# Kernel tuning notes

Hardware: AMD Instinct MI355X
Metric: run time of the kernel (lower is better)

The kernel has to match this reference:

```python
import jax, jax.numpy as jnp
import numpy as np

N_NODES = 100000
N_EDGES = 1600000
D_IN = 128
D_HID = 128


def setup_inputs() -> dict:
    key = jax.random.key(0)
    ks = jax.random.split(key, 9)
    x = jax.random.normal(ks[0], (N_NODES, D_IN), dtype=jnp.float32)
    edge_index = jax.random.randint(ks[1], (2, N_EDGES), 0, N_NODES, dtype=jnp.int64)
    s = 1.0 / np.sqrt(D_IN)
    W0 = jax.random.uniform(ks[2], (D_IN, D_HID), jnp.float32, -s, s)
    W1 = jax.random.uniform(ks[3], (D_HID, D_HID), jnp.float32, -s, s)
    W2 = jax.random.uniform(ks[4], (D_HID, D_HID), jnp.float32, -s, s)
    b0 = jax.random.uniform(ks[5], (D_HID,), jnp.float32, -s, s)
    b1 = jax.random.uniform(ks[6], (D_HID,), jnp.float32, -s, s)
    b2 = jax.random.uniform(ks[7], (D_HID,), jnp.float32, -s, s)
    return {"x": x, "edge_index": edge_index,
            "W0": W0, "W1": W1, "W2": W2, "b0": b0, "b1": b1, "b2": b2}


def _gcn_norm(edge_index, num_nodes):
    # add self loops, compute symmetric normalization D^-1/2 (A+I) D^-1/2
    loop = jnp.arange(num_nodes, dtype=edge_index.dtype)
    src = jnp.concatenate([edge_index[0], loop])
    dst = jnp.concatenate([edge_index[1], loop])
    deg = jax.ops.segment_sum(jnp.ones_like(dst, dtype=jnp.float32), dst,
                              num_segments=num_nodes)
    dis = jnp.where(deg > 0, jax.lax.rsqrt(deg), 0.0)
    norm = dis[src] * dis[dst]  # [E+N]
    return src, dst, norm


def _gcn_conv(x, src, dst, norm, W, b, num_nodes):
    h = x @ W                           # [N, D]
    msg = h[src] * norm[:, None]        # [E+N, D]
    out = jax.ops.segment_sum(msg, dst, num_segments=num_nodes)
    return out + b


def reference(x, edge_index, W0, W1, W2, b0, b1, b2):
    n = x.shape[0]
    src, dst, norm = _gcn_norm(edge_index, n)
    h = jax.nn.relu(_gcn_conv(x, src, dst, norm, W0, b0, n))
    h = jax.nn.relu(_gcn_conv(h, src, dst, norm, W1, b1, n))
    h = jax.nn.relu(_gcn_conv(h, src, dst, norm, W2, b2, n))
    return jax.nn.log_softmax(h, axis=1)
```

## Files before the change

### kernel.cpp

```cpp
#include <hip/hip_runtime.h>
#include <cstdint>


#define D 128
#define NBMAX 800
#define QCAP 4608
#define CB 256

typedef __attribute__((ext_vector_type(8))) short bf16x8;
typedef __attribute__((ext_vector_type(4))) float f32x4;

__device__ inline ushort f_to_bf(float f) {
    uint x = __float_as_uint(f);
    return (ushort)((x + 0x7fffu + ((x >> 16) & 1u)) >> 16);
}
__device__ inline uint pack_bf2(float a, float b) {
    return (uint)f_to_bf(a) | ((uint)f_to_bf(b) << 16);
}
__device__ inline float bf_lo(uint u) { return __uint_as_float(u << 16); }
__device__ inline float bf_hi(uint u) { return __uint_as_float(u & 0xffff0000u); }


__global__ void hist_pass(const int* __restrict__ ei, int* __restrict__ hist,
                          int* __restrict__ cursor, int E, int NB) {
    __shared__ int lh[NBMAX];
    if (blockIdx.x == 0 && threadIdx.x == 0) *cursor = 0;
    for (int i = threadIdx.x; i < NB; i += 256) lh[i] = 0;
    __syncthreads();
    int CE = (E + CB - 1) / CB;
    int e0 = blockIdx.x * CE, e1 = min(e0 + CE, E);
    for (int e = e0 + threadIdx.x; e < e1; e += 256)
        atomicAdd(&lh[ei[(size_t)E + e] >> 7], 1);
    __syncthreads();
    int* hrow = hist + (size_t)blockIdx.x * NB;
    for (int i = threadIdx.x; i < NB; i += 256) hrow[i] = lh[i];
}

__global__ void col_scan(int* __restrict__ hist, int* __restrict__ btotal,
                         int* __restrict__ bbase, int* __restrict__ cursor, int NB) {
    __shared__ int s[256];
    int g = blockIdx.x, t = threadIdx.x;
    int v = hist[(size_t)t * NB + g];
    s[t] = v;
    __syncthreads();
    for (int off = 1; off < 256; off <<= 1) {
        int u = (t >= off) ? s[t - off] : 0;
        __syncthreads();
        s[t] += u;
        __syncthreads();
    }
    hist[(size_t)t * NB + g] = s[t] - v;
    if (t == 255) { btotal[g] = s[255]; bbase[g] = atomicAdd(cursor, s[255]); }
}

__global__ void scatter_pass(const int* __restrict__ ei, const int* __restrict__ hist,
                             const int* __restrict__ bbase, uint* __restrict__ queue,
                             int E, int NB) {
    __shared__ int loff[NBMAX];
    const int* hrow = hist + (size_t)blockIdx.x * NB;
    for (int i = threadIdx.x; i < NB; i += 256) loff[i] = bbase[i] + hrow[i];
    __syncthreads();
    int CE = (E + CB - 1) / CB;
    int e0 = blockIdx.x * CE, e1 = min(e0 + CE, E);
    for (int e = e0 + threadIdx.x; e < e1; e += 256) {
        int d = ei[(size_t)E + e];
        int s = ei[e];
        int slot = atomicAdd(&loff[d >> 7], 1);
        queue[slot] = ((uint)(d & 127) << 17) | (uint)s;
    }
}

__global__ void finalize_pass(const uint* __restrict__ queue, const int* __restrict__ bbase,
                              const int* __restrict__ btotal, int2* __restrict__ bd,
                              float* __restrict__ dis, int* __restrict__ col, int N) {
    __shared__ uint qs[QCAP];
    __shared__ int cnt[128], pre[128], run[128];
    int g = blockIdx.x, t = threadIdx.x;
    int base = bbase[g], m = btotal[g];
    bool fits = (m <= QCAP);
    if (t < 128) { cnt[t] = 0; run[t] = 0; }
    __syncthreads();
    for (int i = t; i < m; i += 256) {
        uint e = queue[base + i];
        if (fits) qs[i] = e;
        atomicAdd(&cnt[e >> 17], 1);
    }
    __syncthreads();
    if (t < 128) pre[t] = cnt[t];
    __syncthreads();
    for (int off = 1; off < 128; off <<= 1) {
        int u = (t < 128 && t >= off) ? pre[t - off] : 0;
        __syncthreads();
        if (t < 128) pre[t] += u;
        __syncthreads();
    }
    if (t < 128) {
        int node = (g << 7) + t;
        if (node < N) {
            bd[node] = make_int2(base + pre[t] - cnt[t], cnt[t]);
            dis[node] = rsqrtf((float)(cnt[t] + 1));
        }
    }
    __syncthreads();
    for (int i = t; i < m; i += 256) {
        uint e = fits ? qs[i] : queue[base + i];
        int idx = (int)(e >> 17);
        int r = atomicAdd(&run[idx], 1);
        col[base + pre[idx] - cnt[idx] + r] = (int)(e & 0x1FFFFu);
    }
}

__global__ void convert_w3(const float* __restrict__ W0, const float* __restrict__ W1,
                           const float* __restrict__ W2, ushort* __restrict__ Wt0,
                           ushort* __restrict__ Wt1, ushort* __restrict__ Wt2) {
    int which = blockIdx.x >> 6;
    int i = (blockIdx.x & 63) * 256 + threadIdx.x;
    const float* W = which == 0 ? W0 : (which == 1 ? W1 : W2);
    ushort* Wt = which == 0 ? Wt0 : (which == 1 ? Wt1 : Wt2);
    int k = i >> 7, nn = i & 127;
    Wt[nn * D + k] = f_to_bf(W[i]);
}

template <int F32IN>
__global__ __launch_bounds__(256)
void gemm_mfma(const void* __restrict__ Xv, const ushort* __restrict__ Wt,
               const float* __restrict__ dis, ushort* __restrict__ G, int n) {
    __shared__ ushort Bs[32 * 64 * 8];
    int tid = threadIdx.x;
    int wave = tid >> 6, lane = tid & 63;
    int lr = lane & 15, quad = lane >> 4;
    int rowbase = blockIdx.x * 128 + wave * 32;

    for (int s = tid; s < 2048; s += 256) {
        int g = s >> 6, l = s & 63;
        int kk = g >> 3, nt = g & 7;
        int srow = nt * 16 + (l & 15);
        int scol = kk * 32 + (l >> 4) * 8;
        ((uint4*)Bs)[s] = *(const uint4*)(Wt + srow * D + scol);
    }
    __syncthreads();

    int ar0 = min(rowbase + lr, n - 1);
    int ar1 = min(rowbase + 16 + lr, n - 1);

    f32x4 acc[2][8];
#pragma unroll
    for (int rt = 0; rt < 2; rt++)
#pragma unroll
        for (int nt = 0; nt < 8; nt++) acc[rt][nt] = (f32x4){0.f, 0.f, 0.f, 0.f};

#pragma unroll
    for (int kk = 0; kk < 4; kk++) {
        bf16x8 a0, a1;
        if (F32IN) {
            const float* X = (const float*)Xv;
            const float* p0 = X + (size_t)ar0 * D + kk * 32 + quad * 8;
            const float* p1 = X + (size_t)ar1 * D + kk * 32 + quad * 8;
            float4 u0 = ((const float4*)p0)[0], v0 = ((const float4*)p0)[1];
            float4 u1 = ((const float4*)p1)[0], v1 = ((const float4*)p1)[1];
            a0 = (bf16x8){(short)f_to_bf(u0.x), (short)f_to_bf(u0.y), (short)f_to_bf(u0.z), (short)f_to_bf(u0.w),
                          (short)f_to_bf(v0.x), (short)f_to_bf(v0.y), (short)f_to_bf(v0.z), (short)f_to_bf(v0.w)};
            a1 = (bf16x8){(short)f_to_bf(u1.x), (short)f_to_bf(u1.y), (short)f_to_bf(u1.z), (short)f_to_bf(u1.w),
                          (short)f_to_bf(v1.x), (short)f_to_bf(v1.y), (short)f_to_bf(v1.z), (short)f_to_bf(v1.w)};
        } else {
            const ushort* X = (const ushort*)Xv;
            a0 = ((const bf16x8*)(X + (size_t)ar0 * D))[kk * 4 + quad];
            a1 = ((const bf16x8*)(X + (size_t)ar1 * D))[kk * 4 + quad];
        }
#pragma unroll
        for (int nt = 0; nt < 8; nt++) {
            bf16x8 b = ((const bf16x8*)Bs)[(kk * 8 + nt) * 64 + lane];
            acc[0][nt] = __builtin_amdgcn_mfma_f32_16x16x32_bf16(a0, b, acc[0][nt], 0, 0, 0);
            acc[1][nt] = __builtin_amdgcn_mfma_f32_16x16x32_bf16(a1, b, acc[1][nt], 0, 0, 0);
        }
    }

#pragma unroll
    for (int rt = 0; rt < 2; rt++) {
#pragma unroll
        for (int r = 0; r < 4; r++) {
            int row = rowbase + rt * 16 + quad * 4 + r;
            if (row < n) {
                float dsc = dis[row];
#pragma unroll
                for (int nt = 0; nt < 8; nt++)
                    G[(size_t)row * D + nt * 16 + lr] = f_to_bf(dsc * acc[rt][nt][r]);
            }
        }
    }
}

__global__ __launch_bounds__(256)
void agg_gemm(const ushort* __restrict__ Gv, const float* __restrict__ dis,
              const int2* __restrict__ bd, const int* __restrict__ col,
              const float* __restrict__ bias, const ushort* __restrict__ Wt,
              ushort* __restrict__ Gout, int n) {
    __shared__ ushort As[16 * 128];
    int tid = threadIdx.x;
    int r16 = tid >> 4, lane16 = tid & 15;
    int node = blockIdx.x * 16 + r16;

    float a0 = 0.f, a1 = 0.f, a2 = 0.f, a3 = 0.f,
          a4 = 0.f, a5 = 0.f, a6 = 0.f, a7 = 0.f;
    if (node < n) {
        const uint4* base = (const uint4*)Gv;
        uint4 u = base[(size_t)node * 16 + lane16];
        a0 = bf_lo(u.x); a1 = bf_hi(u.x); a2 = bf_lo(u.y); a3 = bf_hi(u.y);
        a4 = bf_lo(u.z); a5 = bf_hi(u.z); a6 = bf_lo(u.w); a7 = bf_hi(u.w);

        int2 be = bd[node];
        int beg = be.x, end = be.x + be.y;
        int j = beg;
        for (; j + 8 <= end; j += 8) {
            uint4 v0 = base[(size_t)col[j + 0] * 16 + lane16];
            uint4 v1 = base[(size_t)col[j + 1] * 16 + lane16];
            uint4 v2 = base[(size_t)col[j + 2] * 16 + lane16];
            uint4 v3 = base[(size_t)col[j + 3] * 16 + lane16];
            uint4 v4 = base[(size_t)col[j + 4] * 16 + lane16];
            uint4 v5 = base[(size_t)col[j + 5] * 16 + lane16];
            uint4 v6 = base[(size_t)col[j + 6] * 16 + lane16];
            uint4 v7 = base[(size_t)col[j + 7] * 16 + lane16];
            a0 += bf_lo(v0.x) + bf_lo(v1.x) + bf_lo(v2.x) + bf_lo(v3.x)
                + bf_lo(v4.x) + bf_lo(v5.x) + bf_lo(v6.x) + bf_lo(v7.x);
            a1 += bf_hi(v0.x) + bf_hi(v1.x) + bf_hi(v2.x) + bf_hi(v3.x)
                + bf_hi(v4.x) + bf_hi(v5.x) + bf_hi(v6.x) + bf_hi(v7.x);
            a2 += bf_lo(v0.y) + bf_lo(v1.y) + bf_lo(v2.y) + bf_lo(v3.y)
                + bf_lo(v4.y) + bf_lo(v5.y) + bf_lo(v6.y) + bf_lo(v7.y);
            a3 += bf_hi(v0.y) + bf_hi(v1.y) + bf_hi(v2.y) + bf_hi(v3.y)
                + bf_hi(v4.y) + bf_hi(v5.y) + bf_hi(v6.y) + bf_hi(v7.y);
            a4 += bf_lo(v0.z) + bf_lo(v1.z) + bf_lo(v2.z) + bf_lo(v3.z)
                + bf_lo(v4.z) + bf_lo(v5.z) + bf_lo(v6.z) + bf_lo(v7.z);
            a5 += bf_hi(v0.z) + bf_hi(v1.z) + bf_hi(v2.z) + bf_hi(v3.z)
                + bf_hi(v4.z) + bf_hi(v5.z) + bf_hi(v6.z) + bf_hi(v7.z);
            a6 += bf_lo(v0.w) + bf_lo(v1.w) + bf_lo(v2.w) + bf_lo(v3.w)
                + bf_lo(v4.w) + bf_lo(v5.w) + bf_lo(v6.w) + bf_lo(v7.w);
            a7 += bf_hi(v0.w) + bf_hi(v1.w) + bf_hi(v2.w) + bf_hi(v3.w)
                + bf_hi(v4.w) + bf_hi(v5.w) + bf_hi(v6.w) + bf_hi(v7.w);
        }
        for (; j < end; j++) {
            uint4 v = base[(size_t)col[j] * 16 + lane16];
            a0 += bf_lo(v.x); a1 += bf_hi(v.x); a2 += bf_lo(v.y); a3 += bf_hi(v.y);
            a4 += bf_lo(v.z); a5 += bf_hi(v.z); a6 += bf_lo(v.w); a7 += bf_hi(v.w);
        }

        float di = dis[node];
        float4 bA = ((const float4*)bias)[lane16 * 2];
        float4 bB = ((const float4*)bias)[lane16 * 2 + 1];
        a0 = fmaxf(di * a0 + bA.x, 0.f); a1 = fmaxf(di * a1 + bA.y, 0.f);
        a2 = fmaxf(di * a2 + bA.z, 0.f); a3 = fmaxf(di * a3 + bA.w, 0.f);
        a4 = fmaxf(di * a4 + bB.x, 0.f); a5 = fmaxf(di * a5 + bB.y, 0.f);
        a6 = fmaxf(di * a6 + bB.z, 0.f); a7 = fmaxf(di * a7 + bB.w, 0.f);
    }

    {
        uint4 packed = make_uint4(pack_bf2(a0, a1), pack_bf2(a2, a3),
                                  pack_bf2(a4, a5), pack_bf2(a6, a7));
        uint woff = ((uint)(r16 * 256 + lane16 * 16)) ^ ((uint)(r16 & 7) << 4);
        *(uint4*)((char*)As + woff) = packed;
    }
    __syncthreads();

    int wave = tid >> 6, lane = tid & 63;
    int lr = lane & 15, quad = lane >> 4;
    f32x4 acc0 = (f32x4){0.f, 0.f, 0.f, 0.f};
    f32x4 acc1 = (f32x4){0.f, 0.f, 0.f, 0.f};
    const ushort* wb0 = Wt + ((wave * 2 + 0) * 16 + lr) * D + quad * 8;
    const ushort* wb1 = Wt + ((wave * 2 + 1) * 16 + lr) * D + quad * 8;
#pragma unroll
    for (int kk = 0; kk < 4; kk++) {
        uint roff = ((uint)(lr * 256 + (kk * 4 + quad) * 16)) ^ ((uint)(lr & 7) << 4);
        bf16x8 a = *(const bf16x8*)((const char*)As + roff);
        bf16x8 b0 = *(const bf16x8*)(wb0 + kk * 32);
        bf16x8 b1 = *(const bf16x8*)(wb1 + kk * 32);
        acc0 = __builtin_amdgcn_mfma_f32_16x16x32_bf16(a, b0, acc0, 0, 0, 0);
        acc1 = __builtin_amdgcn_mfma_f32_16x16x32_bf16(a, b1, acc1, 0, 0, 0);
    }

#pragma unroll
    for (int r = 0; r < 4; r++) {
        int row = blockIdx.x * 16 + quad * 4 + r;
        if (row < n) {
            float dsc = dis[row];
            Gout[(size_t)row * D + (wave * 2 + 0) * 16 + lr] = f_to_bf(dsc * acc0[r]);
            Gout[(size_t)row * D + (wave * 2 + 1) * 16 + lr] = f_to_bf(dsc * acc1[r]);
        }
    }
}

template <int MODE>
__global__ __launch_bounds__(256)
void aggregate(const ushort* __restrict__ Gv, const float* __restrict__ dis,
               const int2* __restrict__ bd, const int* __restrict__ col,
               const float* __restrict__ bias, void* __restrict__ outv, int n) {
    int node = blockIdx.x * 16 + (threadIdx.x >> 4);
    if (node >= n) return;
    int lane = threadIdx.x & 15;
    const uint4* base = (const uint4*)Gv;

    uint4 u = base[(size_t)node * 16 + lane];
    float a0 = bf_lo(u.x), a1 = bf_hi(u.x), a2 = bf_lo(u.y), a3 = bf_hi(u.y);
    float a4 = bf_lo(u.z), a5 = bf_hi(u.z), a6 = bf_lo(u.w), a7 = bf_hi(u.w);

    int2 be = bd[node];
    int beg = be.x, end = be.x + be.y;
    int j = beg;
    for (; j + 8 <= end; j += 8) {
        uint4 v0 = base[(size_t)col[j + 0] * 16 + lane];
        uint4 v1 = base[(size_t)col[j + 1] * 16 + lane];
        uint4 v2 = base[(size_t)col[j + 2] * 16 + lane];
        uint4 v3 = base[(size_t)col[j + 3] * 16 + lane];
        uint4 v4 = base[(size_t)col[j + 4] * 16 + lane];
        uint4 v5 = base[(size_t)col[j + 5] * 16 + lane];
        uint4 v6 = base[(size_t)col[j + 6] * 16 + lane];
        uint4 v7 = base[(size_t)col[j + 7] * 16 + lane];
        a0 += bf_lo(v0.x) + bf_lo(v1.x) + bf_lo(v2.x) + bf_lo(v3.x)
            + bf_lo(v4.x) + bf_lo(v5.x) + bf_lo(v6.x) + bf_lo(v7.x);
        a1 += bf_hi(v0.x) + bf_hi(v1.x) + bf_hi(v2.x) + bf_hi(v3.x)
            + bf_hi(v4.x) + bf_hi(v5.x) + bf_hi(v6.x) + bf_hi(v7.x);
        a2 += bf_lo(v0.y) + bf_lo(v1.y) + bf_lo(v2.y) + bf_lo(v3.y)
            + bf_lo(v4.y) + bf_lo(v5.y) + bf_lo(v6.y) + bf_lo(v7.y);
        a3 += bf_hi(v0.y) + bf_hi(v1.y) + bf_hi(v2.y) + bf_hi(v3.y)
            + bf_hi(v4.y) + bf_hi(v5.y) + bf_hi(v6.y) + bf_hi(v7.y);
        a4 += bf_lo(v0.z) + bf_lo(v1.z) + bf_lo(v2.z) + bf_lo(v3.z)
            + bf_lo(v4.z) + bf_lo(v5.z) + bf_lo(v6.z) + bf_lo(v7.z);
        a5 += bf_hi(v0.z) + bf_hi(v1.z) + bf_hi(v2.z) + bf_hi(v3.z)
            + bf_hi(v4.z) + bf_hi(v5.z) + bf_hi(v6.z) + bf_hi(v7.z);
        a6 += bf_lo(v0.w) + bf_lo(v1.w) + bf_lo(v2.w) + bf_lo(v3.w)
            + bf_lo(v4.w) + bf_lo(v5.w) + bf_lo(v6.w) + bf_lo(v7.w);
        a7 += bf_hi(v0.w) + bf_hi(v1.w) + bf_hi(v2.w) + bf_hi(v3.w)
            + bf_hi(v4.w) + bf_hi(v5.w) + bf_hi(v6.w) + bf_hi(v7.w);
    }
    for (; j < end; j++) {
        uint4 v = base[(size_t)col[j] * 16 + lane];
        a0 += bf_lo(v.x); a1 += bf_hi(v.x); a2 += bf_lo(v.y); a3 += bf_hi(v.y);
        a4 += bf_lo(v.z); a5 += bf_hi(v.z); a6 += bf_lo(v.w); a7 += bf_hi(v.w);
    }

    float di = dis[node];
    float4 bA = ((const float4*)bias)[lane * 2];
    float4 bB = ((const float4*)bias)[lane * 2 + 1];
    a0 = fmaxf(di * a0 + bA.x, 0.f); a1 = fmaxf(di * a1 + bA.y, 0.f);
    a2 = fmaxf(di * a2 + bA.z, 0.f); a3 = fmaxf(di * a3 + bA.w, 0.f);
    a4 = fmaxf(di * a4 + bB.x, 0.f); a5 = fmaxf(di * a5 + bB.y, 0.f);
    a6 = fmaxf(di * a6 + bB.z, 0.f); a7 = fmaxf(di * a7 + bB.w, 0.f);

    if (MODE == 1) {
        float m = fmaxf(fmaxf(fmaxf(a0, a1), fmaxf(a2, a3)),
                        fmaxf(fmaxf(a4, a5), fmaxf(a6, a7)));
        for (int off = 8; off > 0; off >>= 1) m = fmaxf(m, __shfl_xor(m, off, 16));
        float e = __expf(a0 - m) + __expf(a1 - m) + __expf(a2 - m) + __expf(a3 - m)
                + __expf(a4 - m) + __expf(a5 - m) + __expf(a6 - m) + __expf(a7 - m);
        for (int off = 8; off > 0; off >>= 1) e += __shfl_xor(e, off, 16);
        float ls = m + __logf(e);
        ((float4*)outv)[(size_t)node * 32 + lane * 2]     = make_float4(a0 - ls, a1 - ls, a2 - ls, a3 - ls);
        ((float4*)outv)[(size_t)node * 32 + lane * 2 + 1] = make_float4(a4 - ls, a5 - ls, a6 - ls, a7 - ls);
    } else {
        ((uint4*)outv)[(size_t)node * 16 + lane] =
            make_uint4(pack_bf2(a0, a1), pack_bf2(a2, a3), pack_bf2(a4, a5), pack_bf2(a6, a7));
    }
}


static inline size_t align256(size_t x) { return (x + 255) & ~(size_t)255; }

extern "C" void kernel_launch(void* const* d_in, const int* in_sizes, int n_in,
                              void* d_out, int out_size, void* d_ws, size_t ws_size,
                              hipStream_t stream) {
    const float* x  = (const float*)d_in[0];
    const int*   ei = (const int*)d_in[1];
    const float* W0 = (const float*)d_in[2];
    const float* W1 = (const float*)d_in[3];
    const float* W2 = (const float*)d_in[4];
    const float* b0 = (const float*)d_in[5];
    const float* b1 = (const float*)d_in[6];
    const float* b2 = (const float*)d_in[7];
    float* out      = (float*)d_out;

    const int N = in_sizes[0] / D;
    const int E = in_sizes[1] / 2;
    const int NB = (N + 127) >> 7;

    char* ws = (char*)d_ws;
    size_t off = 0;
    float*  dis      = (float*)(ws + off);  off = align256(off + (size_t)N * 4);
    int2*   bd       = (int2*)(ws + off);   off = align256(off + (size_t)N * 8);
    int*    hist     = (int*)(ws + off);    off = align256(off + (size_t)CB * NB * 4);
    int*    btotal   = (int*)(ws + off);    off = align256(off + (size_t)NB * 4);
    int*    bbase    = (int*)(ws + off);    off = align256(off + (size_t)NB * 4);
    int*    cursor   = (int*)(ws + off);    off = align256(off + 4);
    ushort* Wt0      = (ushort*)(ws + off); off = align256(off + (size_t)D * D * 2);
    ushort* Wt1      = (ushort*)(ws + off); off = align256(off + (size_t)D * D * 2);
    ushort* Wt2      = (ushort*)(ws + off); off = align256(off + (size_t)D * D * 2);
    int*    col      = (int*)(ws + off);    off = align256(off + (size_t)E * 4);
    ushort* bufA     = (ushort*)(ws + off); off = align256(off + (size_t)N * D * 2);
    ushort* bufB     = (ushort*)(ws + off); off = align256(off + (size_t)N * D * 2);
    uint*   queue    = (uint*)bufB;
    (void)ws_size;

    hist_pass<<<CB, 256, 0, stream>>>(ei, hist, cursor, E, NB);
    col_scan<<<NB, 256, 0, stream>>>(hist, btotal, bbase, cursor, NB);
    scatter_pass<<<CB, 256, 0, stream>>>(ei, hist, bbase, queue, E, NB);
    finalize_pass<<<NB, 256, 0, stream>>>(queue, bbase, btotal, bd, dis, col, N);

    convert_w3<<<192, 256, 0, stream>>>(W0, W1, W2, Wt0, Wt1, Wt2);

    const int gemmBlocks = (N + 127) / 128;
    const int fuseBlocks = (N + 15) / 16;

    gemm_mfma<1><<<gemmBlocks, 256, 0, stream>>>(x, Wt0, dis, bufA, N);
    agg_gemm<<<fuseBlocks, 256, 0, stream>>>(bufA, dis, bd, col, b0, Wt1, bufB, N);
    agg_gemm<<<fuseBlocks, 256, 0, stream>>>(bufB, dis, bd, col, b1, Wt2, bufA, N);
    aggregate<1><<<fuseBlocks, 256, 0, stream>>>(bufA, dis, bd, col, b2, out, N);
}
```

Baseline: 422.9 us.

## Unfuse aggregate-gemm, merge weight conversion into histogram, widen histogram chunks

Replaces the fused agg_gemm kernels with separate aggregate and gemm_mfma launches for each layer, using the output buffer as scratch for intermediate bf16 features. Folds the weight transpose/convert kernel into the histogram kernel as extra blocks to save a launch. Triples the number of histogram/scatter chunks and makes col_scan handle three rows per thread. Unfusing adds two launches and an extra round-trip of the intermediate features through memory, in exchange for a larger-tile GEMM and a plain aggregation kernel.

```diff
diff --git a/kernel.cpp b/kernel.cpp
--- a/kernel.cpp
+++ b/kernel.cpp
@@ -5,7 +5,7 @@
 #define D 128
 #define NBMAX 800
 #define QCAP 4608
-#define CB 256
+#define CB 768
 
 typedef __attribute__((ext_vector_type(8))) short bf16x8;
 typedef __attribute__((ext_vector_type(4))) float f32x4;
@@ -21,18 +21,31 @@
 __device__ inline float bf_hi(uint u) { return __uint_as_float(u & 0xffff0000u); }
 
 
-__global__ void hist_pass(const int* __restrict__ ei, int* __restrict__ hist,
-                          int* __restrict__ cursor, int E, int NB) {
+__global__ void hist_conv(const int* __restrict__ ei, int* __restrict__ hist,
+                          int* __restrict__ cursor, int E, int NB,
+                          const float* __restrict__ W0, const float* __restrict__ W1,
+                          const float* __restrict__ W2, ushort* __restrict__ Wt0,
+                          ushort* __restrict__ Wt1, ushort* __restrict__ Wt2) {
+    int b = blockIdx.x;
+    if (b >= CB) {
+        int bb = b - CB;
+        int which = bb >> 6;
+        int i = (bb & 63) * 256 + threadIdx.x;
+        const float* W = which == 0 ? W0 : (which == 1 ? W1 : W2);
+        ushort* Wt = which == 0 ? Wt0 : (which == 1 ? Wt1 : Wt2);
+        Wt[(i & 127) * D + (i >> 7)] = f_to_bf(W[i]);
+        return;
+    }
     __shared__ int lh[NBMAX];
-    if (blockIdx.x == 0 && threadIdx.x == 0) *cursor = 0;
+    if (b == 0 && threadIdx.x == 0) *cursor = 0;
     for (int i = threadIdx.x; i < NB; i += 256) lh[i] = 0;
     __syncthreads();
     int CE = (E + CB - 1) / CB;
-    int e0 = blockIdx.x * CE, e1 = min(e0 + CE, E);
+    int e0 = b * CE, e1 = min(e0 + CE, E);
     for (int e = e0 + threadIdx.x; e < e1; e += 256)
         atomicAdd(&lh[ei[(size_t)E + e] >> 7], 1);
     __syncthreads();
-    int* hrow = hist + (size_t)blockIdx.x * NB;
+    int* hrow = hist + (size_t)b * NB;
     for (int i = threadIdx.x; i < NB; i += 256) hrow[i] = lh[i];
 }
 
@@ -40,8 +53,14 @@
                          int* __restrict__ bbase, int* __restrict__ cursor, int NB) {
     __shared__ int s[256];
     int g = blockIdx.x, t = threadIdx.x;
-    int v = hist[(size_t)t * NB + g];
-    s[t] = v;
+    int v[3];
+    int sum = 0;
+#pragma unroll
+    for (int i = 0; i < 3; i++) {
+        v[i] = hist[(size_t)(t * 3 + i) * NB + g];
+        sum += v[i];
+    }
+    s[t] = sum;
     __syncthreads();
     for (int off = 1; off < 256; off <<= 1) {
         int u = (t >= off) ? s[t - off] : 0;
@@ -49,7 +68,12 @@
         s[t] += u;
         __syncthreads();
     }
-    hist[(size_t)t * NB + g] = s[t] - v;
+    int excl = s[t] - sum;
+#pragma unroll
+    for (int i = 0; i < 3; i++) {
+        hist[(size_t)(t * 3 + i) * NB + g] = excl;
+        excl += v[i];
+    }
     if (t == 255) { btotal[g] = s[255]; bbase[g] = atomicAdd(cursor, s[255]); }
 }
 
@@ -108,17 +132,6 @@
         int r = atomicAdd(&run[idx], 1);
         col[base + pre[idx] - cnt[idx] + r] = (int)(e & 0x1FFFFu);
     }
-}
-
-__global__ void convert_w3(const float* __restrict__ W0, const float* __restrict__ W1,
-                           const float* __restrict__ W2, ushort* __restrict__ Wt0,
-                           ushort* __restrict__ Wt1, ushort* __restrict__ Wt2) {
-    int which = blockIdx.x >> 6;
-    int i = (blockIdx.x & 63) * 256 + threadIdx.x;
-    const float* W = which == 0 ? W0 : (which == 1 ? W1 : W2);
-    ushort* Wt = which == 0 ? Wt0 : (which == 1 ? Wt1 : Wt2);
-    int k = i >> 7, nn = i & 127;
-    Wt[nn * D + k] = f_to_bf(W[i]);
 }
 
 template <int F32IN>
@@ -186,103 +199,6 @@
                 for (int nt = 0; nt < 8; nt++)
                     G[(size_t)row * D + nt * 16 + lr] = f_to_bf(dsc * acc[rt][nt][r]);
             }
-        }
-    }
-}
-
-__global__ __launch_bounds__(256)
-void agg_gemm(const ushort* __restrict__ Gv, const float* __restrict__ dis,
-              const int2* __restrict__ bd, const int* __restrict__ col,
-              const float* __restrict__ bias, const ushort* __restrict__ Wt,
-              ushort* __restrict__ Gout, int n) {
-    __shared__ ushort As[16 * 128];
-    int tid = threadIdx.x;
-    int r16 = tid >> 4, lane16 = tid & 15;
-    int node = blockIdx.x * 16 + r16;
-
-    float a0 = 0.f, a1 = 0.f, a2 = 0.f, a3 = 0.f,
-          a4 = 0.f, a5 = 0.f, a6 = 0.f, a7 = 0.f;
-    if (node < n) {
-        const uint4* base = (const uint4*)Gv;
-        uint4 u = base[(size_t)node * 16 + lane16];
-        a0 = bf_lo(u.x); a1 = bf_hi(u.x); a2 = bf_lo(u.y); a3 = bf_hi(u.y);
-        a4 = bf_lo(u.z); a5 = bf_hi(u.z); a6 = bf_lo(u.w); a7 = bf_hi(u.w);
-
-        int2 be = bd[node];
-        int beg = be.x, end = be.x + be.y;
-        int j = beg;
-        for (; j + 8 <= end; j += 8) {
-            uint4 v0 = base[(size_t)col[j + 0] * 16 + lane16];
-            uint4 v1 = base[(size_t)col[j + 1] * 16 + lane16];
-            uint4 v2 = base[(size_t)col[j + 2] * 16 + lane16];
-            uint4 v3 = base[(size_t)col[j + 3] * 16 + lane16];
-            uint4 v4 = base[(size_t)col[j + 4] * 16 + lane16];
-            uint4 v5 = base[(size_t)col[j + 5] * 16 + lane16];
-            uint4 v6 = base[(size_t)col[j + 6] * 16 + lane16];
-            uint4 v7 = base[(size_t)col[j + 7] * 16 + lane16];
-            a0 += bf_lo(v0.x) + bf_lo(v1.x) + bf_lo(v2.x) + bf_lo(v3.x)
-                + bf_lo(v4.x) + bf_lo(v5.x) + bf_lo(v6.x) + bf_lo(v7.x);
-            a1 += bf_hi(v0.x) + bf_hi(v1.x) + bf_hi(v2.x) + bf_hi(v3.x)
-                + bf_hi(v4.x) + bf_hi(v5.x) + bf_hi(v6.x) + bf_hi(v7.x);
-            a2 += bf_lo(v0.y) + bf_lo(v1.y) + bf_lo(v2.y) + bf_lo(v3.y)
-                + bf_lo(v4.y) + bf_lo(v5.y) + bf_lo(v6.y) + bf_lo(v7.y);
-            a3 += bf_hi(v0.y) + bf_hi(v1.y) + bf_hi(v2.y) + bf_hi(v3.y)
-                + bf_hi(v4.y) + bf_hi(v5.y) + bf_hi(v6.y) + bf_hi(v7.y);
-            a4 += bf_lo(v0.z) + bf_lo(v1.z) + bf_lo(v2.z) + bf_lo(v3.z)
-                + bf_lo(v4.z) + bf_lo(v5.z) + bf_lo(v6.z) + bf_lo(v7.z);
-            a5 += bf_hi(v0.z) + bf_hi(v1.z) + bf_hi(v2.z) + bf_hi(v3.z)
-                + bf_hi(v4.z) + bf_hi(v5.z) + bf_hi(v6.z) + bf_hi(v7.z);
-            a6 += bf_lo(v0.w) + bf_lo(v1.w) + bf_lo(v2.w) + bf_lo(v3.w)
-                + bf_lo(v4.w) + bf_lo(v5.w) + bf_lo(v6.w) + bf_lo(v7.w);
-            a7 += bf_hi(v0.w) + bf_hi(v1.w) + bf_hi(v2.w) + bf_hi(v3.w)
-                + bf_hi(v4.w) + bf_hi(v5.w) + bf_hi(v6.w) + bf_hi(v7.w);
-        }
-        for (; j < end; j++) {
-            uint4 v = base[(size_t)col[j] * 16 + lane16];
-            a0 += bf_lo(v.x); a1 += bf_hi(v.x); a2 += bf_lo(v.y); a3 += bf_hi(v.y);
-            a4 += bf_lo(v.z); a5 += bf_hi(v.z); a6 += bf_lo(v.w); a7 += bf_hi(v.w);
-        }
-
-        float di = dis[node];
-        float4 bA = ((const float4*)bias)[lane16 * 2];
-        float4 bB = ((const float4*)bias)[lane16 * 2 + 1];
-        a0 = fmaxf(di * a0 + bA.x, 0.f); a1 = fmaxf(di * a1 + bA.y, 0.f);
-        a2 = fmaxf(di * a2 + bA.z, 0.f); a3 = fmaxf(di * a3 + bA.w, 0.f);
-        a4 = fmaxf(di * a4 + bB.x, 0.f); a5 = fmaxf(di * a5 + bB.y, 0.f);
-        a6 = fmaxf(di * a6 + bB.z, 0.f); a7 = fmaxf(di * a7 + bB.w, 0.f);
-    }
-
-    {
-        uint4 packed = make_uint4(pack_bf2(a0, a1), pack_bf2(a2, a3),
-                                  pack_bf2(a4, a5), pack_bf2(a6, a7));
-        uint woff = ((uint)(r16 * 256 + lane16 * 16)) ^ ((uint)(r16 & 7) << 4);
-        *(uint4*)((char*)As + woff) = packed;
-    }
-    __syncthreads();
-
-    int wave = tid >> 6, lane = tid & 63;
-    int lr = lane & 15, quad = lane >> 4;
-    f32x4 acc0 = (f32x4){0.f, 0.f, 0.f, 0.f};
-    f32x4 acc1 = (f32x4){0.f, 0.f, 0.f, 0.f};
-    const ushort* wb0 = Wt + ((wave * 2 + 0) * 16 + lr) * D + quad * 8;
-    const ushort* wb1 = Wt + ((wave * 2 + 1) * 16 + lr) * D + quad * 8;
-#pragma unroll
-    for (int kk = 0; kk < 4; kk++) {
-        uint roff = ((uint)(lr * 256 + (kk * 4 + quad) * 16)) ^ ((uint)(lr & 7) << 4);
-        bf16x8 a = *(const bf16x8*)((const char*)As + roff);
-        bf16x8 b0 = *(const bf16x8*)(wb0 + kk * 32);
-        bf16x8 b1 = *(const bf16x8*)(wb1 + kk * 32);
-        acc0 = __builtin_amdgcn_mfma_f32_16x16x32_bf16(a, b0, acc0, 0, 0, 0);
-        acc1 = __builtin_amdgcn_mfma_f32_16x16x32_bf16(a, b1, acc1, 0, 0, 0);
-    }
-
-#pragma unroll
-    for (int r = 0; r < 4; r++) {
-        int row = blockIdx.x * 16 + quad * 4 + r;
-        if (row < n) {
-            float dsc = dis[row];
-            Gout[(size_t)row * D + (wave * 2 + 0) * 16 + lr] = f_to_bf(dsc * acc0[r]);
-            Gout[(size_t)row * D + (wave * 2 + 1) * 16 + lr] = f_to_bf(dsc * acc1[r]);
         }
     }
 }
@@ -394,21 +310,23 @@
     int*    col      = (int*)(ws + off);    off = align256(off + (size_t)E * 4);
     ushort* bufA     = (ushort*)(ws + off); off = align256(off + (size_t)N * D * 2);
     ushort* bufB     = (ushort*)(ws + off); off = align256(off + (size_t)N * D * 2);
+    ushort* dhead    = (ushort*)d_out;
     uint*   queue    = (uint*)bufB;
     (void)ws_size;
 
-    hist_pass<<<CB, 256, 0, stream>>>(ei, hist, cursor, E, NB);
+    hist_conv<<<CB + 192, 256, 0, stream>>>(ei, hist, cursor, E, NB,
+                                            W0, W1, W2, Wt0, Wt1, Wt2);
     col_scan<<<NB, 256, 0, stream>>>(hist, btotal, bbase, cursor, NB);
     scatter_pass<<<CB, 256, 0, stream>>>(ei, hist, bbase, queue, E, NB);
     finalize_pass<<<NB, 256, 0, stream>>>(queue, bbase, btotal, bd, dis, col, N);
 
-    convert_w3<<<192, 256, 0, stream>>>(W0, W1, W2, Wt0, Wt1, Wt2);
-
     const int gemmBlocks = (N + 127) / 128;
-    const int fuseBlocks = (N + 15) / 16;
-
-    gemm_mfma<1><<<gemmBlocks, 256, 0, stream>>>(x, Wt0, dis, bufA, N);
-    agg_gemm<<<fuseBlocks, 256, 0, stream>>>(bufA, dis, bd, col, b0, Wt1, bufB, N);
-    agg_gemm<<<fuseBlocks, 256, 0, stream>>>(bufB, dis, bd, col, b1, Wt2, bufA, N);
-    aggregate<1><<<fuseBlocks, 256, 0, stream>>>(bufA, dis, bd, col, b2, out, N);
-}
+    const int aggBlocks  = (N + 15) / 16;
+
+    gemm_mfma<1><<<gemmBlocks, 256, 0, stream>>>(x, Wt0, dis, dhead, N);
+    aggregate<0><<<aggBlocks, 256, 0, stream>>>(dhead, dis, bd, col, b0, bufA, N);
+    gemm_mfma<0><<<gemmBlocks, 256, 0, stream>>>(bufA, Wt1, dis, bufB, N);
+    aggregate<0><<<aggBlocks, 256, 0, stream>>>(bufB, dis, bd, col, b1, dhead, N);
+    gemm_mfma<0><<<gemmBlocks, 256, 0, stream>>>(dhead, Wt2, dis, bufA, N);
+    aggregate<1><<<aggBlocks, 256, 0, stream>>>(bufA, dis, bd, col, b2, out, N);
+}
```

New measurement: 412.8 us, median of 2. -2.4%, faster.
